# Kernel tuning notes

Hardware: AMD Instinct MI355X
Metric: run time of the kernel (lower is better)

Reference implementation:

```python
import jax, jax.numpy as jnp
import numpy as np

N = 50000
E = 800000
F = 128


def gcn_smooth(edge_index, x):
    """Symmetric-normalized GCN smoothing: D^-1/2 (A + I) D^-1/2 x.

    edge_index: [2, E] int (src, dst) of a sparse graph; self-loops added here.
    x: [N, F] float node features.
    """
    src, dst = edge_index[0], edge_index[1]
    n = x.shape[0]
    # degree of A + I
    deg = jax.ops.segment_sum(jnp.ones((src.shape[0],), x.dtype), dst, num_segments=n) + 1.0
    dinv = jax.lax.rsqrt(deg)  # [N]
    # per-edge normalization d^-1/2[src] * d^-1/2[dst]
    norm_e = dinv[src] * dinv[dst]  # [E]
    msg = x[src] * norm_e[:, None]  # [E, F] -- gather + scale
    agg = jax.ops.segment_sum(msg, dst, num_segments=n)  # scatter-add over dst
    # self-loop contribution: dinv[i]^2 * x[i]
    return agg + (dinv * dinv)[:, None] * x


def setup_inputs() -> dict:
    key = jax.random.key(0)
    ks = jax.random.split(key, 12)
    inp = {
        "X_HypGNet": jax.random.normal(ks[0], (N, F), jnp.float32),
        "X_CGNet": jax.random.normal(ks[1], (N, F), jnp.float32),
        "X_SGNet": jax.random.normal(ks[2], (N, F), jnp.float32),
        "edge_index_hyp": jax.random.randint(ks[3], (2, E), 0, N, dtype=jnp.int32),
        "edge_index_c": jax.random.randint(ks[4], (2, E), 0, N, dtype=jnp.int32),
        "edge_index_s": jax.random.randint(ks[5], (2, E), 0, N, dtype=jnp.int32),
        "W_hyp": jax.random.normal(ks[6], (F, F), jnp.float32) * 0.05,
        "b_hyp": jax.random.normal(ks[7], (F,), jnp.float32) * 0.05,
        "W_cg": jax.random.normal(ks[8], (F, F), jnp.float32) * 0.05,
        "b_cg": jax.random.normal(ks[9], (F,), jnp.float32) * 0.05,
        "W_sg": jax.random.normal(ks[10], (F, F), jnp.float32) * 0.05,
        "b_sg": jax.random.normal(ks[11], (F,), jnp.float32) * 0.05,
    }
    return inp


def reference(X_HypGNet, X_CGNet, X_SGNet, edge_index_hyp, edge_index_c, edge_index_s,
              W_hyp, b_hyp, W_cg, b_cg, W_sg, b_sg):
    X_hyp = X_HypGNet @ W_hyp + b_hyp
    X_cg = X_CGNet @ W_cg + b_cg
    X_sg = X_SGNet @ W_sg + b_sg
    X_hyp_s = gcn_smooth(edge_index_hyp, X_hyp)
    X_cg_s = gcn_smooth(edge_index_c, X_cg)
    X_sg_s = gcn_smooth(edge_index_s, X_sg)
    return (X_hyp_s, X_cg_s, X_sg_s)
```

## Files before the change

### kernel.cpp

```cpp
#include <hip/hip_runtime.h>

#define F_DIM 128
#define NG 3
#define AEPT 16
#define CAP 48
#define MAXBIN 256
#define SPILL_CAP 8192

typedef __attribute__((ext_vector_type(8))) short short8_t;
typedef __attribute__((ext_vector_type(4))) float f32x4;

__device__ __forceinline__ unsigned short f2bf(float f) {
    unsigned int x = __float_as_uint(f);
    unsigned int r = x + 0x7fffu + ((x >> 16) & 1u);
    return (unsigned short)(r >> 16);
}
__device__ __forceinline__ float bflo(unsigned int u) { return __uint_as_float(u << 16); }
__device__ __forceinline__ float bfhi(unsigned int u) { return __uint_as_float(u & 0xffff0000u); }

__device__ __forceinline__ short8_t cvt8(float4 x0, float4 x1) {
    union { short8_t s; uint4 u; } pk;
    pk.u.x = (unsigned)f2bf(x0.x) | ((unsigned)f2bf(x0.y) << 16);
    pk.u.y = (unsigned)f2bf(x0.z) | ((unsigned)f2bf(x0.w) << 16);
    pk.u.z = (unsigned)f2bf(x1.x) | ((unsigned)f2bf(x1.y) << 16);
    pk.u.w = (unsigned)f2bf(x1.z) | ((unsigned)f2bf(x1.w) << 16);
    return pk.s;
}

struct GArgs {
    const int* src[NG]; const int* dst[NG];
    const float* X[NG]; const float* W[NG]; const float* b[NG];
    float* out[NG];
    unsigned short* Xps[NG];
    unsigned short* sorted[NG];
    unsigned short* Wtb[NG];
    int* binbuf[NG];
    int* bincur[NG];
    int* cstore[NG];
    float* dinv[NG];
    int* spill[NG];
    int* spill_n[NG];
    int nbin, bincap;
};

__global__ __launch_bounds__(256) void init_kernel(GArgs a, int g0) {
    int g = g0 + blockIdx.y;
    for (int i = threadIdx.x; i < a.nbin; i += 256) a.bincur[g][i] = i * a.bincap;
    if (threadIdx.x == 0) a.spill_n[g][0] = 0;
    const float* W = a.W[g];
    unsigned short* Wtb = a.Wtb[g];
    for (int i = threadIdx.x; i < 16 * 128; i += 256) {
        int kg = i >> 7, c = i & 127;
        const float* wp = W + (size_t)(kg * 8) * F_DIM + c;
        uint4 pk;
        pk.x = (unsigned)f2bf(wp[0])   | ((unsigned)f2bf(wp[128]) << 16);
        pk.y = (unsigned)f2bf(wp[256]) | ((unsigned)f2bf(wp[384]) << 16);
        pk.z = (unsigned)f2bf(wp[512]) | ((unsigned)f2bf(wp[640]) << 16);
        pk.w = (unsigned)f2bf(wp[768]) | ((unsigned)f2bf(wp[896]) << 16);
        *(uint4*)(Wtb + (size_t)i * 8) = pk;
    }
}

__global__ __launch_bounds__(256) void work_kernel(GArgs a, int g0, int E, int n, int gA) {
    int g = g0 + blockIdx.y;
    const int t = threadIdx.x;
    if ((int)blockIdx.x < gA) {
        __shared__ int cnt[MAXBIN];
        __shared__ int lcur[MAXBIN];
        const int nbin = a.nbin, bincap = a.bincap;
        for (int i = t; i < nbin; i += 256) cnt[i] = 0;
        __syncthreads();
        const int* dst = a.dst[g];
        const int* src = a.src[g];
        const int base = blockIdx.x * (256 * AEPT) + t;
        int dd[AEPT], sv[AEPT];
#pragma unroll
        for (int i = 0; i < AEPT; ++i) {
            int e = base + i * 256;
            int ec = (e < E) ? e : 0;
            dd[i] = __builtin_nontemporal_load(&dst[ec]);
            sv[i] = __builtin_nontemporal_load(&src[ec]);
            if (e < E) atomicAdd(&cnt[dd[i] >> 8], 1);
        }
        __syncthreads();
        for (int i = t; i < nbin; i += 256) {
            int c = cnt[i];
            lcur[i] = c ? atomicAdd(&a.bincur[g][i], c) : 0;
        }
        __syncthreads();
        int* binbuf = a.binbuf[g];
#pragma unroll
        for (int i = 0; i < AEPT; ++i) {
            int e = base + i * 256;
            if (e < E) {
                int bin = dd[i] >> 8;
                int pos = atomicAdd(&lcur[bin], 1);
                if (pos < (bin + 1) * bincap) {
                    binbuf[pos] = ((dd[i] & 255) << 16) | sv[i];
                } else {
                    int sp = atomicAdd(a.spill_n[g], 1);
                    if (sp < SPILL_CAP) {
                        a.spill[g][2 * sp] = sv[i];
                        a.spill[g][2 * sp + 1] = dd[i];
                    }
                }
            }
        }
    } else {
        const int bx = blockIdx.x - gA;
        const int l = t & 63;
        const int wv = t >> 6;
        const int wr = wv >> 1, wc = wv & 1;
        const int lm = l & 15, lk = l >> 4;
        const int rowA = bx * 128 + wr * 64 + lm;
        const float* X = a.X[g];
        const unsigned short* Wtb = a.Wtb[g];

        f32x4 acc[4][4] = {};
#pragma unroll
        for (int ks = 0; ks < 4; ++ks) {
            short8_t bv[4];
#pragma unroll
            for (int nt = 0; nt < 4; ++nt) {
                int col = wc * 64 + nt * 16 + lm;
                bv[nt] = *(const short8_t*)(Wtb + ((size_t)((ks * 4 + lk) * 128 + col)) * 8);
            }
            float4 xr[4][2];
#pragma unroll
            for (int mt = 0; mt < 4; ++mt) {
                int row = rowA + mt * 16;
                row = row < n ? row : n - 1;
                const float4* xp = (const float4*)(X + (size_t)row * F_DIM + ks * 32 + lk * 8);
                xr[mt][0] = xp[0];
                xr[mt][1] = xp[1];
            }
#pragma unroll
            for (int mt = 0; mt < 4; ++mt) {
                short8_t af = cvt8(xr[mt][0], xr[mt][1]);
#pragma unroll
                for (int nt = 0; nt < 4; ++nt)
                    acc[mt][nt] = __builtin_amdgcn_mfma_f32_16x16x32_bf16(af, bv[nt],
                                                                          acc[mt][nt], 0, 0, 0);
            }
        }

        const float* bia = a.b[g];
        unsigned short* Xps = a.Xps[g];
        const int rb = bx * 128 + wr * 64;
#pragma unroll
        for (int nt = 0; nt < 4; ++nt) {
            int col = wc * 64 + nt * 16 + lm;
            float bc = bia[col];
#pragma unroll
            for (int mt = 0; mt < 4; ++mt) {
                int rbase = rb + mt * 16 + lk * 4;
#pragma unroll
                for (int r = 0; r < 4; ++r) {
                    int row = rbase + r;
                    if (row < n)
                        Xps[(size_t)row * F_DIM + col] = f2bf(acc[mt][nt][r] + bc);
                }
            }
        }
    }
}

__global__ __launch_bounds__(256) void binB_kernel(GArgs a, int g0, int n) {
    int g = g0 + blockIdx.y;
    int bin = blockIdx.x;
    const int t = threadIdx.x;
    __shared__ int cnt[256];
    cnt[t] = 0;
    __syncthreads();
    const int bincap = a.bincap;
    int used = a.bincur[g][bin] - bin * bincap;
    int rd = min(used, bincap);
    const int* bb = a.binbuf[g] + bin * bincap;
    unsigned short* sorted = a.sorted[g];
    for (int j = t; j < rd; j += 256) {
        int u = bb[j];
        int dl = u >> 16;
        int s = u & 0xffff;
        int tk = atomicAdd(&cnt[dl], 1);
        int d = (bin << 8) + dl;
        if (tk < CAP) {
            sorted[d * CAP + tk] = (unsigned short)s;
        } else {
            int sp = atomicAdd(a.spill_n[g], 1);
            if (sp < SPILL_CAP) {
                a.spill[g][2 * sp] = s;
                a.spill[g][2 * sp + 1] = d;
            }
        }
    }
    __syncthreads();
    int d = (bin << 8) + t;
    if (d < n) {
        int deg = cnt[t];
        a.cstore[g][d] = min(deg, CAP);
        a.dinv[g][d] = rsqrtf((float)deg + 1.0f);
    }
}

__global__ __launch_bounds__(256) void agg_kernel(GArgs a, int g0, int n) {
    int g = g0 + blockIdx.y;
    int wave = (blockIdx.x * 256 + threadIdx.x) >> 6;
    if (wave >= n) return;
    const int l = threadIdx.x & 63;
    const int c = l & 15;
    const int hi = l >> 4;
    const uint4* Xp4 = (const uint4*)a.Xps[g];
    const unsigned short* sorted = a.sorted[g];
    const float* dinv = a.dinv[g];
    int cnt = a.cstore[g][wave];
    int s = 0;
    float dv = 0.f;
    if (l < cnt) {
        s = (int)__builtin_nontemporal_load(&sorted[(size_t)wave * CAP + l]);
        dv = dinv[s];
    }
    float a0 = 0.f, a1 = 0.f, a2 = 0.f, a3 = 0.f, a4 = 0.f, a5 = 0.f, a6 = 0.f, a7 = 0.f;
    for (int k = 0; k < cnt; k += 16) {
        int e0 = k + hi, e1 = k + 4 + hi, e2 = k + 8 + hi, e3 = k + 12 + hi;
        int s0 = __shfl(s, e0, 64);
        int s1 = __shfl(s, e1, 64);
        int s2 = __shfl(s, e2, 64);
        int s3 = __shfl(s, e3, 64);
        float w0 = __shfl(dv, e0, 64);
        float w1 = __shfl(dv, e1, 64);
        float w2 = __shfl(dv, e2, 64);
        float w3 = __shfl(dv, e3, 64);
        uint4 v0 = Xp4[(size_t)s0 * 16 + c];
        uint4 v1 = Xp4[(size_t)s1 * 16 + c];
        uint4 v2 = Xp4[(size_t)s2 * 16 + c];
        uint4 v3 = Xp4[(size_t)s3 * 16 + c];
        if (e0 >= cnt) w0 = 0.f;
        if (e1 >= cnt) w1 = 0.f;
        if (e2 >= cnt) w2 = 0.f;
        if (e3 >= cnt) w3 = 0.f;
        a0 += bflo(v0.x) * w0; a1 += bfhi(v0.x) * w0;
        a2 += bflo(v0.y) * w0; a3 += bfhi(v0.y) * w0;
        a4 += bflo(v0.z) * w0; a5 += bfhi(v0.z) * w0;
        a6 += bflo(v0.w) * w0; a7 += bfhi(v0.w) * w0;
        a0 += bflo(v1.x) * w1; a1 += bfhi(v1.x) * w1;
        a2 += bflo(v1.y) * w1; a3 += bfhi(v1.y) * w1;
        a4 += bflo(v1.z) * w1; a5 += bfhi(v1.z) * w1;
        a6 += bflo(v1.w) * w1; a7 += bfhi(v1.w) * w1;
        a0 += bflo(v2.x) * w2; a1 += bfhi(v2.x) * w2;
        a2 += bflo(v2.y) * w2; a3 += bfhi(v2.y) * w2;
        a4 += bflo(v2.z) * w2; a5 += bfhi(v2.z) * w2;
        a6 += bflo(v2.w) * w2; a7 += bfhi(v2.w) * w2;
        a0 += bflo(v3.x) * w3; a1 += bfhi(v3.x) * w3;
        a2 += bflo(v3.y) * w3; a3 += bfhi(v3.y) * w3;
        a4 += bflo(v3.z) * w3; a5 += bfhi(v3.z) * w3;
        a6 += bflo(v3.w) * w3; a7 += bfhi(v3.w) * w3;
    }
    a0 += __shfl_xor(a0, 16, 64); a0 += __shfl_xor(a0, 32, 64);
    a1 += __shfl_xor(a1, 16, 64); a1 += __shfl_xor(a1, 32, 64);
    a2 += __shfl_xor(a2, 16, 64); a2 += __shfl_xor(a2, 32, 64);
    a3 += __shfl_xor(a3, 16, 64); a3 += __shfl_xor(a3, 32, 64);
    a4 += __shfl_xor(a4, 16, 64); a4 += __shfl_xor(a4, 32, 64);
    a5 += __shfl_xor(a5, 16, 64); a5 += __shfl_xor(a5, 32, 64);
    a6 += __shfl_xor(a6, 16, 64); a6 += __shfl_xor(a6, 32, 64);
    a7 += __shfl_xor(a7, 16, 64); a7 += __shfl_xor(a7, 32, 64);
    float dd = dinv[wave];
    uint4 v = Xp4[(size_t)wave * 16 + c];
    a0 += bflo(v.x) * dd; a1 += bfhi(v.x) * dd;
    a2 += bflo(v.y) * dd; a3 += bfhi(v.y) * dd;
    a4 += bflo(v.z) * dd; a5 += bfhi(v.z) * dd;
    a6 += bflo(v.w) * dd; a7 += bfhi(v.w) * dd;
    if (hi == 0) {
        float* o = (float*)a.out[g] + (size_t)wave * F_DIM + c * 8;
        *(float4*)(o + 0) = make_float4(a0 * dd, a1 * dd, a2 * dd, a3 * dd);
        *(float4*)(o + 4) = make_float4(a4 * dd, a5 * dd, a6 * dd, a7 * dd);
    }
}

__global__ __launch_bounds__(128) void spill_kernel(GArgs a, int g0) {
    int g = g0 + blockIdx.y;
    int ns = min(a.spill_n[g][0], SPILL_CAP);
    const unsigned short* Xps = a.Xps[g];
    const float* dinv = a.dinv[g];
    float* out = a.out[g];
    for (int i = blockIdx.x; i < ns; i += gridDim.x) {
        int s = a.spill[g][2 * i];
        int d = a.spill[g][2 * i + 1];
        float w = dinv[d] * dinv[s];
        int f = threadIdx.x;
        float v = __uint_as_float(((unsigned int)Xps[(size_t)s * F_DIM + f]) << 16);
        unsafeAtomicAdd(&out[(size_t)d * F_DIM + f], w * v);
    }
}

extern "C" void kernel_launch(void* const* d_in, const int* in_sizes, int n_in,
                              void* d_out, int out_size, void* d_ws, size_t ws_size,
                              hipStream_t stream) {
    const float* Xin[NG] = {(const float*)d_in[0], (const float*)d_in[1], (const float*)d_in[2]};
    const int* ei[NG] = {(const int*)d_in[3], (const int*)d_in[4], (const int*)d_in[5]};
    const float* Wk[NG] = {(const float*)d_in[6], (const float*)d_in[8], (const float*)d_in[10]};
    const float* bk[NG] = {(const float*)d_in[7], (const float*)d_in[9], (const float*)d_in[11]};

    const int N = in_sizes[0] / F_DIM;
    const int E = in_sizes[3] / 2;
    float* out = (float*)d_out;

    const int nbin = (N + 255) >> 8;
    const int bincap = E / nbin + E / (3 * nbin) + 256;

    const size_t xps_b = (size_t)N * F_DIM * 2;
    const size_t sorted_b = (size_t)N * CAP * 2;
    const size_t wtb_b = (size_t)16 * 128 * 8 * 2;
    const size_t binbuf_b = (size_t)nbin * bincap * 4;
    const size_t nb = (size_t)N * 4;
    const size_t bincur_b = ((size_t)nbin * 4 + 255) / 256 * 256;
    const size_t spill_b = (size_t)SPILL_CAP * 8 + 64;
    const size_t per = ((xps_b + sorted_b + wtb_b + binbuf_b + 2 * nb + bincur_b + spill_b
                         + 255) / 256) * 256;
    const bool fused = ws_size >= (size_t)NG * per;
    char* base = (char*)d_ws;

    GArgs a;
    a.nbin = nbin;
    a.bincap = bincap;
    for (int r = 0; r < NG; ++r) {
        char* s = base + (size_t)(fused ? r : 0) * per;
        size_t off = 0;
        a.Xps[r] = (unsigned short*)(s + off); off += xps_b;
        a.sorted[r] = (unsigned short*)(s + off); off += sorted_b;
        a.Wtb[r] = (unsigned short*)(s + off); off += wtb_b;
        a.binbuf[r] = (int*)(s + off); off += binbuf_b;
        a.cstore[r] = (int*)(s + off); off += nb;
        a.dinv[r] = (float*)(s + off); off += nb;
        a.bincur[r] = (int*)(s + off); off += bincur_b;
        a.spill[r] = (int*)(s + off);
        a.spill_n[r] = (int*)(s + off + spill_b - 64);
        a.src[r] = ei[r];
        a.dst[r] = ei[r] + E;
        a.X[r] = Xin[r];
        a.W[r] = Wk[r];
        a.b[r] = bk[r];
        a.out[r] = out + (size_t)r * N * F_DIM;
    }

    const dim3 blk(256);
    const int gAe = (E + 256 * AEPT - 1) / (256 * AEPT);
    const int gR = (N + 127) / 128;
    const int gG = (N * 64 + 255) / 256;

    if (fused) {
        init_kernel<<<dim3(1, NG), blk, 0, stream>>>(a, 0);
        work_kernel<<<dim3(gAe + gR, NG), blk, 0, stream>>>(a, 0, E, N, gAe);
        binB_kernel<<<dim3(nbin, NG), blk, 0, stream>>>(a, 0, N);
        agg_kernel<<<dim3(gG, NG), blk, 0, stream>>>(a, 0, N);
        spill_kernel<<<dim3(16, NG), dim3(128), 0, stream>>>(a, 0);
    } else {
        for (int g = 0; g < NG; ++g) {
            init_kernel<<<dim3(1, 1), blk, 0, stream>>>(a, g);
            work_kernel<<<dim3(gAe + gR, 1), blk, 0, stream>>>(a, g, E, N, gAe);
            binB_kernel<<<dim3(nbin, 1), blk, 0, stream>>>(a, g, N);
            agg_kernel<<<dim3(gG, 1), blk, 0, stream>>>(a, g, N);
            spill_kernel<<<dim3(16, 1), dim3(128), 0, stream>>>(a, g);
        }
    }
}
```

Measured before the change: 176.8 us.

## Split binning and GEMM into separate kernels, store projected features as fp16

Splits the combined work_kernel into a binning kernel and a standalone GEMM kernel, launched after binB. The GEMM tile shrinks from 128 to 64 rows per block, which doubles the grid. The intermediate projected features are stored as fp16 instead of bf16, and the aggregation and spill paths convert them back with fp16 casts. The intent is to cut register pressure and the divergent-role overhead of the fused kernel and to gain mantissa precision. The cost is one extra kernel launch and the loss of overlap between binning and the GEMM.

```diff
diff --git a/kernel.cpp b/kernel.cpp
--- a/kernel.cpp
+++ b/kernel.cpp
@@ -9,14 +9,13 @@
 
 typedef __attribute__((ext_vector_type(8))) short short8_t;
 typedef __attribute__((ext_vector_type(4))) float f32x4;
+typedef _Float16 h2 __attribute__((ext_vector_type(2)));
 
 __device__ __forceinline__ unsigned short f2bf(float f) {
     unsigned int x = __float_as_uint(f);
     unsigned int r = x + 0x7fffu + ((x >> 16) & 1u);
     return (unsigned short)(r >> 16);
 }
-__device__ __forceinline__ float bflo(unsigned int u) { return __uint_as_float(u << 16); }
-__device__ __forceinline__ float bfhi(unsigned int u) { return __uint_as_float(u & 0xffff0000u); }
 
 __device__ __forceinline__ short8_t cvt8(float4 x0, float4 x1) {
     union { short8_t s; uint4 u; } pk;
@@ -61,104 +60,46 @@
     }
 }
 
-__global__ __launch_bounds__(256) void work_kernel(GArgs a, int g0, int E, int n, int gA) {
-    int g = g0 + blockIdx.y;
+__global__ __launch_bounds__(256) void binA_kernel(GArgs a, int g0, int E) {
+    int g = g0 + blockIdx.y;
+    __shared__ int cnt[MAXBIN];
+    __shared__ int lcur[MAXBIN];
     const int t = threadIdx.x;
-    if ((int)blockIdx.x < gA) {
-        __shared__ int cnt[MAXBIN];
-        __shared__ int lcur[MAXBIN];
-        const int nbin = a.nbin, bincap = a.bincap;
-        for (int i = t; i < nbin; i += 256) cnt[i] = 0;
-        __syncthreads();
-        const int* dst = a.dst[g];
-        const int* src = a.src[g];
-        const int base = blockIdx.x * (256 * AEPT) + t;
-        int dd[AEPT], sv[AEPT];
-#pragma unroll
-        for (int i = 0; i < AEPT; ++i) {
-            int e = base + i * 256;
-            int ec = (e < E) ? e : 0;
-            dd[i] = __builtin_nontemporal_load(&dst[ec]);
-            sv[i] = __builtin_nontemporal_load(&src[ec]);
-            if (e < E) atomicAdd(&cnt[dd[i] >> 8], 1);
-        }
-        __syncthreads();
-        for (int i = t; i < nbin; i += 256) {
-            int c = cnt[i];
-            lcur[i] = c ? atomicAdd(&a.bincur[g][i], c) : 0;
-        }
-        __syncthreads();
-        int* binbuf = a.binbuf[g];
-#pragma unroll
-        for (int i = 0; i < AEPT; ++i) {
-            int e = base + i * 256;
-            if (e < E) {
-                int bin = dd[i] >> 8;
-                int pos = atomicAdd(&lcur[bin], 1);
-                if (pos < (bin + 1) * bincap) {
-                    binbuf[pos] = ((dd[i] & 255) << 16) | sv[i];
-                } else {
-                    int sp = atomicAdd(a.spill_n[g], 1);
-                    if (sp < SPILL_CAP) {
-                        a.spill[g][2 * sp] = sv[i];
-                        a.spill[g][2 * sp + 1] = dd[i];
-                    }
-                }
-            }
-        }
-    } else {
-        const int bx = blockIdx.x - gA;
-        const int l = t & 63;
-        const int wv = t >> 6;
-        const int wr = wv >> 1, wc = wv & 1;
-        const int lm = l & 15, lk = l >> 4;
-        const int rowA = bx * 128 + wr * 64 + lm;
-        const float* X = a.X[g];
-        const unsigned short* Wtb = a.Wtb[g];
-
-        f32x4 acc[4][4] = {};
-#pragma unroll
-        for (int ks = 0; ks < 4; ++ks) {
-            short8_t bv[4];
-#pragma unroll
-            for (int nt = 0; nt < 4; ++nt) {
-                int col = wc * 64 + nt * 16 + lm;
-                bv[nt] = *(const short8_t*)(Wtb + ((size_t)((ks * 4 + lk) * 128 + col)) * 8);
-            }
-            float4 xr[4][2];
-#pragma unroll
-            for (int mt = 0; mt < 4; ++mt) {
-                int row = rowA + mt * 16;
-                row = row < n ? row : n - 1;
-                const float4* xp = (const float4*)(X + (size_t)row * F_DIM + ks * 32 + lk * 8);
-                xr[mt][0] = xp[0];
-                xr[mt][1] = xp[1];
-            }
-#pragma unroll
-            for (int mt = 0; mt < 4; ++mt) {
-                short8_t af = cvt8(xr[mt][0], xr[mt][1]);
-#pragma unroll
-                for (int nt = 0; nt < 4; ++nt)
-                    acc[mt][nt] = __builtin_amdgcn_mfma_f32_16x16x32_bf16(af, bv[nt],
-                                                                          acc[mt][nt], 0, 0, 0);
-            }
-        }
-
-        const float* bia = a.b[g];
-        unsigned short* Xps = a.Xps[g];
-        const int rb = bx * 128 + wr * 64;
-#pragma unroll
-        for (int nt = 0; nt < 4; ++nt) {
-            int col = wc * 64 + nt * 16 + lm;
-            float bc = bia[col];
-#pragma unroll
-            for (int mt = 0; mt < 4; ++mt) {
-                int rbase = rb + mt * 16 + lk * 4;
-#pragma unroll
-                for (int r = 0; r < 4; ++r) {
-                    int row = rbase + r;
-                    if (row < n)
-                        Xps[(size_t)row * F_DIM + col] = f2bf(acc[mt][nt][r] + bc);
+    const int nbin = a.nbin, bincap = a.bincap;
+    for (int i = t; i < nbin; i += 256) cnt[i] = 0;
+    __syncthreads();
+    const int* dst = a.dst[g];
+    const int* src = a.src[g];
+    const int base = blockIdx.x * (256 * AEPT) + t;
+    int dd[AEPT], sv[AEPT];
+#pragma unroll
+    for (int i = 0; i < AEPT; ++i) {
+        int e = base + i * 256;
+        int ec = (e < E) ? e : 0;
+        dd[i] = __builtin_nontemporal_load(&dst[ec]);
+        sv[i] = __builtin_nontemporal_load(&src[ec]);
+        if (e < E) atomicAdd(&cnt[dd[i] >> 8], 1);
+    }
+    __syncthreads();
+    for (int i = t; i < nbin; i += 256) {
+        int c = cnt[i];
+        lcur[i] = c ? atomicAdd(&a.bincur[g][i], c) : 0;
+    }
+    __syncthreads();
+    int* binbuf = a.binbuf[g];
+#pragma unroll
+    for (int i = 0; i < AEPT; ++i) {
+        int e = base + i * 256;
+        if (e < E) {
+            int bin = dd[i] >> 8;
+            int pos = atomicAdd(&lcur[bin], 1);
+            if (pos < (bin + 1) * bincap) {
+                binbuf[pos] = ((dd[i] & 255) << 16) | sv[i];
+            } else {
+                int sp = atomicAdd(a.spill_n[g], 1);
+                if (sp < SPILL_CAP) {
+                    a.spill[g][2 * sp] = sv[i];
+                    a.spill[g][2 * sp + 1] = dd[i];
                 }
             }
         }
@@ -202,6 +143,67 @@
     }
 }
 
+__global__ __launch_bounds__(256) void gemm_kernel(GArgs a, int g0, int n) {
+    int g = g0 + blockIdx.y;
+    const int t = threadIdx.x;
+    const int l = t & 63;
+    const int wv = t >> 6;
+    const int wr = wv >> 1, wc = wv & 1;
+    const int lm = l & 15, lk = l >> 4;
+    const int rowA = blockIdx.x * 64 + wr * 32 + lm;
+    const float* X = a.X[g];
+    const unsigned short* Wtb = a.Wtb[g];
+
+    f32x4 acc[2][4] = {};
+#pragma unroll
+    for (int ks = 0; ks < 4; ++ks) {
+        short8_t bv[4];
+#pragma unroll
+        for (int nt = 0; nt < 4; ++nt) {
+            int col = wc * 64 + nt * 16 + lm;
+            bv[nt] = *(const short8_t*)(Wtb + ((size_t)((ks * 4 + lk) * 128 + col)) * 8);
+        }
+        float4 xr[2][2];
+#pragma unroll
+        for (int mt = 0; mt < 2; ++mt) {
+            int row = rowA + mt * 16;
+            row = row < n ? row : n - 1;
+            const float4* xp = (const float4*)(X + (size_t)row * F_DIM + ks * 32 + lk * 8);
+            xr[mt][0] = xp[0];
+            xr[mt][1] = xp[1];
+        }
+#pragma unroll
+        for (int mt = 0; mt < 2; ++mt) {
+            short8_t af = cvt8(xr[mt][0], xr[mt][1]);
+#pragma unroll
+            for (int nt = 0; nt < 4; ++nt)
+                acc[mt][nt] = __builtin_amdgcn_mfma_f32_16x16x32_bf16(af, bv[nt],
+                                                                      acc[mt][nt], 0, 0, 0);
+        }
+    }
+
+    const float* bia = a.b[g];
+    unsigned short* Xps = a.Xps[g];
+    const int rb = blockIdx.x * 64 + wr * 32;
+#pragma unroll
+    for (int nt = 0; nt < 4; ++nt) {
+        int col = wc * 64 + nt * 16 + lm;
+        float bc = bia[col];
+#pragma unroll
+        for (int mt = 0; mt < 2; ++mt) {
+            int rbase = rb + mt * 16 + lk * 4;
+#pragma unroll
+            for (int r = 0; r < 4; ++r) {
+                int row = rbase + r;
+                if (row < n) {
+                    _Float16 h = (_Float16)(acc[mt][nt][r] + bc);
+                    Xps[(size_t)row * F_DIM + col] = __builtin_bit_cast(unsigned short, h);
+                }
+            }
+        }
+    }
+}
+
 __global__ __launch_bounds__(256) void agg_kernel(GArgs a, int g0, int n) {
     int g = g0 + blockIdx.y;
     int wave = (blockIdx.x * 256 + threadIdx.x) >> 6;
@@ -220,6 +222,17 @@
         dv = dinv[s];
     }
     float a0 = 0.f, a1 = 0.f, a2 = 0.f, a3 = 0.f, a4 = 0.f, a5 = 0.f, a6 = 0.f, a7 = 0.f;
+#define ACC8(V, W)                                                                 \
+    {                                                                              \
+        h2 p0 = __builtin_bit_cast(h2, (V).x);                                     \
+        h2 p1 = __builtin_bit_cast(h2, (V).y);                                     \
+        h2 p2 = __builtin_bit_cast(h2, (V).z);                                     \
+        h2 p3 = __builtin_bit_cast(h2, (V).w);                                     \
+        a0 += (float)p0.x * (W); a1 += (float)p0.y * (W);                          \
+        a2 += (float)p1.x * (W); a3 += (float)p1.y * (W);                          \
+        a4 += (float)p2.x * (W); a5 += (float)p2.y * (W);                          \
+        a6 += (float)p3.x * (W); a7 += (float)p3.y * (W);                          \
+    }
     for (int k = 0; k < cnt; k += 16) {
         int e0 = k + hi, e1 = k + 4 + hi, e2 = k + 8 + hi, e3 = k + 12 + hi;
         int s0 = __shfl(s, e0, 64);
@@ -238,22 +251,10 @@
         if (e1 >= cnt) w1 = 0.f;
         if (e2 >= cnt) w2 = 0.f;
         if (e3 >= cnt) w3 = 0.f;
-        a0 += bflo(v0.x) * w0; a1 += bfhi(v0.x) * w0;
-        a2 += bflo(v0.y) * w0; a3 += bfhi(v0.y) * w0;
-        a4 += bflo(v0.z) * w0; a5 += bfhi(v0.z) * w0;
-        a6 += bflo(v0.w) * w0; a7 += bfhi(v0.w) * w0;
-        a0 += bflo(v1.x) * w1; a1 += bfhi(v1.x) * w1;
-        a2 += bflo(v1.y) * w1; a3 += bfhi(v1.y) * w1;
-        a4 += bflo(v1.z) * w1; a5 += bfhi(v1.z) * w1;
-        a6 += bflo(v1.w) * w1; a7 += bfhi(v1.w) * w1;
-        a0 += bflo(v2.x) * w2; a1 += bfhi(v2.x) * w2;
-        a2 += bflo(v2.y) * w2; a3 += bfhi(v2.y) * w2;
-        a4 += bflo(v2.z) * w2; a5 += bfhi(v2.z) * w2;
-        a6 += bflo(v2.w) * w2; a7 += bfhi(v2.w) * w2;
-        a0 += bflo(v3.x) * w3; a1 += bfhi(v3.x) * w3;
-        a2 += bflo(v3.y) * w3; a3 += bfhi(v3.y) * w3;
-        a4 += bflo(v3.z) * w3; a5 += bfhi(v3.z) * w3;
-        a6 += bflo(v3.w) * w3; a7 += bfhi(v3.w) * w3;
+        ACC8(v0, w0)
+        ACC8(v1, w1)
+        ACC8(v2, w2)
+        ACC8(v3, w3)
     }
     a0 += __shfl_xor(a0, 16, 64); a0 += __shfl_xor(a0, 32, 64);
     a1 += __shfl_xor(a1, 16, 64); a1 += __shfl_xor(a1, 32, 64);
@@ -265,10 +266,8 @@
     a7 += __shfl_xor(a7, 16, 64); a7 += __shfl_xor(a7, 32, 64);
     float dd = dinv[wave];
     uint4 v = Xp4[(size_t)wave * 16 + c];
-    a0 += bflo(v.x) * dd; a1 += bfhi(v.x) * dd;
-    a2 += bflo(v.y) * dd; a3 += bfhi(v.y) * dd;
-    a4 += bflo(v.z) * dd; a5 += bfhi(v.z) * dd;
-    a6 += bflo(v.w) * dd; a7 += bfhi(v.w) * dd;
+    ACC8(v, dd)
+#undef ACC8
     if (hi == 0) {
         float* o = (float*)a.out[g] + (size_t)wave * F_DIM + c * 8;
         *(float4*)(o + 0) = make_float4(a0 * dd, a1 * dd, a2 * dd, a3 * dd);
@@ -287,8 +286,8 @@
         int d = a.spill[g][2 * i + 1];
         float w = dinv[d] * dinv[s];
         int f = threadIdx.x;
-        float v = __uint_as_float(((unsigned int)Xps[(size_t)s * F_DIM + f]) << 16);
-        unsafeAtomicAdd(&out[(size_t)d * F_DIM + f], w * v);
+        _Float16 h = __builtin_bit_cast(_Float16, Xps[(size_t)s * F_DIM + f]);
+        unsafeAtomicAdd(&out[(size_t)d * F_DIM + f], w * (float)h);
     }
 }
 
@@ -344,20 +343,22 @@
 
     const dim3 blk(256);
     const int gAe = (E + 256 * AEPT - 1) / (256 * AEPT);
-    const int gR = (N + 127) / 128;
+    const int gR = (N + 63) / 64;
     const int gG = (N * 64 + 255) / 256;
 
     if (fused) {
         init_kernel<<<dim3(1, NG), blk, 0, stream>>>(a, 0);
-        work_kernel<<<dim3(gAe + gR, NG), blk, 0, stream>>>(a, 0, E, N, gAe);
+        binA_kernel<<<dim3(gAe, NG), blk, 0, stream>>>(a, 0, E);
         binB_kernel<<<dim3(nbin, NG), blk, 0, stream>>>(a, 0, N);
+        gemm_kernel<<<dim3(gR, NG), blk, 0, stream>>>(a, 0, N);
         agg_kernel<<<dim3(gG, NG), blk, 0, stream>>>(a, 0, N);
         spill_kernel<<<dim3(16, NG), dim3(128), 0, stream>>>(a, 0);
     } else {
         for (int g = 0; g < NG; ++g) {
             init_kernel<<<dim3(1, 1), blk, 0, stream>>>(a, g);
-            work_kernel<<<dim3(gAe + gR, 1), blk, 0, stream>>>(a, g, E, N, gAe);
+            binA_kernel<<<dim3(gAe, 1), blk, 0, stream>>>(a, g, E);
             binB_kernel<<<dim3(nbin, 1), blk, 0, stream>>>(a, g, N);
+            gemm_kernel<<<dim3(gR, 1), blk, 0, stream>>>(a, g, N);
             agg_kernel<<<dim3(gG, 1), blk, 0, stream>>>(a, g, N);
             spill_kernel<<<dim3(16, 1), dim3(128), 0, stream>>>(a, g);
         }
```

Measured after the change: 175.7 us, median of 2. No clear change (-0.6%).
